# Kernel optimization log

Hardware: AMD Instinct MI355X
Metric: run time of the kernel (lower is better)

## Reference

```python
import jax, jax.numpy as jnp
import numpy as np

T = 5
EPS = 1e-05


def setup_inputs() -> dict:
    key = jax.random.key(0)
    X = jax.random.normal(key, (64, 512, 32, 32), dtype=jnp.float32)
    return {"X": X}


def reference(X):
    # IterNorm (training branch): whiten channels via Newton-Schulz inverse sqrt.
    N, C, H, W = X.shape
    x = jnp.transpose(X, (1, 0, 2, 3)).reshape(C, -1)  # [d, m], d=C, m=N*H*W
    d, m = x.shape
    mean = jnp.mean(x, axis=-1, keepdims=True)
    xc = x - mean
    I = jnp.eye(d, dtype=X.dtype)
    # Sigma = eps*I + (1/m) xc xc^T  (addmm(eps, I, 1/m, xc, xc^T))
    Sigma = EPS * I + (xc @ xc.T) / m
    rTr = 1.0 / jnp.trace(Sigma)          # (Sigma * I).sum().reciprocal()
    Sigma_N = Sigma * rTr
    P = I
    for _ in range(T):
        # P_{k+1} = 1.5*P_k - 0.5 * P_k^3 @ Sigma_N
        P = 1.5 * P - 0.5 * (P @ P @ P) @ Sigma_N
    wm = P * jnp.sqrt(rTr)                # whitening matrix ~ Sigma^{-1/2}
    xn = wm @ xc                          # [d, m]
    Xn = jnp.transpose(xn.reshape(C, N, H, W), (1, 0, 2, 3))
    return Xn
```

## Files before the change

### kernel.cpp

```cpp
#include <hip/hip_runtime.h>
#include <math.h>

#define Nn   64
#define Cc   512
#define HWs  1024
#define CHW  (Cc * HWs)
#define Mm   (Nn * HWs)
#define EPSC 1e-5f
#define NBC  128

typedef unsigned int   u32;
typedef unsigned short u16;
typedef unsigned long long u64;
typedef __attribute__((ext_vector_type(8))) short  short8;
typedef __attribute__((ext_vector_type(4))) float  floatx4;

__device__ __forceinline__ u16 f2bf(float f) {
    u32 u = __float_as_uint(f);
    u += 0x7fff + ((u >> 16) & 1);
    return (u16)(u >> 16);
}
__device__ __forceinline__ float bf2f(u16 h) {
    return __uint_as_float(((u32)h) << 16);
}

__device__ __forceinline__ void gld_lds16(const u16* g, u16* l) {
    __builtin_amdgcn_global_load_lds(
        (const __attribute__((address_space(1))) u32*)g,
        (__attribute__((address_space(3))) u32*)l, 16, 0, 0);
}

#define AUX_SC 0x11

__device__ __forceinline__ void gld_lds16_sc(const u16* g, u16* l) {
    __builtin_amdgcn_global_load_lds(
        (const __attribute__((address_space(1))) u32*)g,
        (__attribute__((address_space(3))) u32*)l, 16, 0, AUX_SC);
}
__device__ __forceinline__ void st8_sc(u16* p, u64 pk) {
    asm volatile("global_store_dwordx2 %0, %1, off sc0 sc1"
                 :: "v"(p), "v"(pk) : "memory");
}
__device__ __forceinline__ u64 pk4(const u16* h) {
    return (u64)h[0] | ((u64)h[1] << 16) | ((u64)h[2] << 32) | ((u64)h[3] << 48);
}

#define WAITV(N) asm volatile("s_waitcnt vmcnt(" #N ")" ::: "memory")
#define RAWBAR() __builtin_amdgcn_s_barrier()

__global__ __launch_bounds__(256) void convert_transpose(const float* __restrict__ X,
                                                         u16* __restrict__ Xbf,
                                                         u16* __restrict__ Xt,
                                                         float* __restrict__ meanP) {
    const int hT = blockIdx.x;
    const int h0 = hT << 6;
    const int c0 = blockIdx.y << 6;
    const int n  = blockIdx.z;
    const int t  = threadIdx.x;
    __shared__ u16   T[64][65];
    __shared__ float red[64][17];

    const float* Xn  = X   + (size_t)n * CHW;
    u16*         Xbn = Xbf + (size_t)n * CHW;
    u16*         Xtn = Xt  + (size_t)n * CHW;

    const int cl = t >> 4;
    const int h4 = (t & 15) << 2;
#pragma unroll
    for (int i = 0; i < 4; ++i) {
        const int c = cl + (i << 4);
        float4 v = *(const float4*)&Xn[(size_t)(c0 + c) * HWs + h0 + h4];
        red[c][t & 15] = v.x + v.y + v.z + v.w;
        u16 b0 = f2bf(v.x), b1 = f2bf(v.y), b2 = f2bf(v.z), b3 = f2bf(v.w);
        *(ushort4*)&Xbn[(size_t)(c0 + c) * HWs + h0 + h4] = make_ushort4(b0, b1, b2, b3);
        T[c][h4]     = b0;
        T[c][h4 + 1] = b1;
        T[c][h4 + 2] = b2;
        T[c][h4 + 3] = b3;
    }
    __syncthreads();
    const int hl = t >> 4;
    const int c4 = (t & 15) << 2;
#pragma unroll
    for (int i = 0; i < 4; ++i) {
        const int h = hl + (i << 4);
        ushort4 pk = make_ushort4(T[c4][h], T[c4 + 1][h], T[c4 + 2][h], T[c4 + 3][h]);
        *(ushort4*)&Xtn[(size_t)(h0 + h) * Cc + c0 + c4] = pk;
    }
    if (t < 64) {
        float s = 0.f;
#pragma unroll
        for (int j = 0; j < 16; ++j) s += red[t][j];
        atomicAdd(&meanP[hT * 512 + c0 + t], s);
    }
}

__global__ __launch_bounds__(256) void gram_mfma(const u16* __restrict__ Xbf,
                                                 float* __restrict__ G) {
    static const int TI[10] = {0,0,0,0,1,1,1,2,2,3};
    static const int TJ[10] = {0,1,2,3,1,2,3,2,3,3};
    const int id = blockIdx.x;
    const int q  = id >> 3;
    const int x  = q % 10;
    const int y  = (id & 7) + ((q / 10) << 3);
    const int i0 = TI[x] << 7;
    const int j0 = TJ[x] << 7;
    const int n0 = y << 1;
    const int t  = threadIdx.x;
    const int w  = t >> 6, l = t & 63;

    __shared__ u16 As[2][4096];
    __shared__ u16 Bs[2][4096];

    floatx4 acc[4][4];
#pragma unroll
    for (int mi = 0; mi < 4; ++mi)
#pragma unroll
        for (int ni = 0; ni < 4; ++ni) acc[mi][ni] = (floatx4){0.f, 0.f, 0.f, 0.f};

    const int lr = l >> 2;
    const int lc = (l & 3) << 3;
    const int wm = w >> 1, wn = w & 1;
    const int fm = l & 15, fq = l >> 4;

    auto issue = [&](int s, int bb) {
        const u16* Xn = Xbf + (size_t)(n0 + (s >> 5)) * CHW;
        const int hw  = (s & 31) << 5;
#pragma unroll
        for (int p = 0; p < 2; ++p) {
            const int g   = w * 2 + p;
            const int row = g * 16 + lr;
            gld_lds16(Xn + (size_t)(i0 + row) * HWs + hw + lc, &As[bb][g * 512]);
            gld_lds16(Xn + (size_t)(j0 + row) * HWs + hw + lc, &Bs[bb][g * 512]);
        }
    };

    issue(0, 0);
    issue(1, 1);
    for (int s = 0; s < 64; ++s) {
        if (s < 63) WAITV(4); else WAITV(0);
        RAWBAR();
        const int bb = s & 1;
        short8 a[4], b[4];
#pragma unroll
        for (int mi = 0; mi < 4; ++mi)
            a[mi] = *(const short8*)&As[bb][(wm * 64 + mi * 16 + fm) * 32 + fq * 8];
#pragma unroll
        for (int ni = 0; ni < 4; ++ni)
            b[ni] = *(const short8*)&Bs[bb][(wn * 64 + ni * 16 + fm) * 32 + fq * 8];
#pragma unroll
        for (int mi = 0; mi < 4; ++mi)
#pragma unroll
            for (int ni = 0; ni < 4; ++ni)
                acc[mi][ni] = __builtin_amdgcn_mfma_f32_16x16x32_bf16(
                    a[mi], b[ni], acc[mi][ni], 0, 0, 0);
        RAWBAR();
        if (s < 62) issue(s + 2, bb);
    }
#pragma unroll
    for (int mi = 0; mi < 4; ++mi)
#pragma unroll
        for (int ni = 0; ni < 4; ++ni)
#pragma unroll
            for (int r = 0; r < 4; ++r) {
                const int gi = i0 + wm * 64 + mi * 16 + fq * 4 + r;
                const int gj = j0 + wn * 64 + ni * 16 + fm;
                atomicAdd(&G[(size_t)gi * Cc + gj], acc[mi][ni][r]);
            }
}

__device__ __forceinline__ void gridbar(int* bar, int gen) {
    asm volatile("s_waitcnt vmcnt(0)" ::: "memory");
    __syncthreads();
    if (threadIdx.x == 0) {
        __hip_atomic_fetch_add(bar, 1, __ATOMIC_RELAXED, __HIP_MEMORY_SCOPE_AGENT);
        while (__hip_atomic_load(bar, __ATOMIC_RELAXED, __HIP_MEMORY_SCOPE_AGENT) < gen * NBC)
            __builtin_amdgcn_s_sleep(1);
    }
    __syncthreads();
}

template <int MR>
__device__ __forceinline__ void mm_bk64(const u16* Ah, const u16* Al,
                                        const u16* Bh, const u16* Bl,
                                        int i0, int j0,
                                        float alpha, const float* D, float beta,
                                        float* Cf, u16* Ch, u16* Cl, u16* S) {
    const int t = threadIdx.x, w = t >> 6, l = t & 63;
    const int wm = w >> 1, wn = w & 1, fm = l & 15, fq = l >> 4;
    const int lr = l >> 2, lc = (l & 3) << 3;
    constexpr int MI     = MR / 32;
    constexpr int OFF_AL = MR * 64;
    constexpr int OFF_BH = 2 * MR * 64;
    constexpr int OFF_BL = 2 * MR * 64 + 4096;
    constexpr int BUFSZ  = 2 * MR * 64 + 8192;

    const u16* src  = (w == 0) ? Ah : (w == 1) ? Al : (w == 2) ? Bh : Bl;
    const int rbase = (w < 2) ? i0 : j0;
    const int R     = (w < 2) ? MR : 64;
    const int OFF   = (w == 0) ? 0 : (w == 1) ? OFF_AL : (w == 2) ? OFF_BH : OFF_BL;

    floatx4 acc[MI][2];
#pragma unroll
    for (int mi = 0; mi < MI; ++mi)
#pragma unroll
        for (int ni = 0; ni < 2; ++ni) acc[mi][ni] = (floatx4){0.f, 0.f, 0.f, 0.f};

    auto issue = [&](int c, int bb) {
        u16* dst = S + bb * BUFSZ + OFF;
        const u16* sp = src + (size_t)rbase * 512 + (c << 6);
#pragma unroll
        for (int s = 0; s < 2; ++s)
#pragma unroll 4
            for (int g = 0; g < (R >> 4); ++g)
                gld_lds16_sc(sp + (size_t)(g * 16 + lr) * 512 + s * 32 + lc,
                             dst + s * R * 32 + g * 512);
    };
    auto waitL = [&](bool last) {
        if (last) { WAITV(0); return; }
        if (MR == 64) { WAITV(8); }
        else if (w < 2) { WAITV(4); } else { WAITV(8); }
    };
    auto compute = [&](int bb) {
        const u16* base = S + bb * BUFSZ;
#pragma unroll
        for (int s = 0; s < 2; ++s) {
            short8 ah[MI], al[MI], bh[2], bl[2];
#pragma unroll
            for (int mi = 0; mi < MI; ++mi) {
                const int r = wm * (MR / 2) + mi * 16 + fm;
                const int o = s * MR * 32 + r * 32 + fq * 8;
                ah[mi] = *(const short8*)&base[o];
                al[mi] = *(const short8*)&base[OFF_AL + o];
            }
#pragma unroll
            for (int ni = 0; ni < 2; ++ni) {
                const int r = wn * 32 + ni * 16 + fm;
                const int o = s * 2048 + r * 32 + fq * 8;
                bh[ni] = *(const short8*)&base[OFF_BH + o];
                bl[ni] = *(const short8*)&base[OFF_BL + o];
            }
#pragma unroll
            for (int mi = 0; mi < MI; ++mi)
#pragma unroll
                for (int ni = 0; ni < 2; ++ni) {
                    acc[mi][ni] = __builtin_amdgcn_mfma_f32_16x16x32_bf16(ah[mi], bh[ni], acc[mi][ni], 0, 0, 0);
                    acc[mi][ni] = __builtin_amdgcn_mfma_f32_16x16x32_bf16(ah[mi], bl[ni], acc[mi][ni], 0, 0, 0);
                    acc[mi][ni] = __builtin_amdgcn_mfma_f32_16x16x32_bf16(al[mi], bh[ni], acc[mi][ni], 0, 0, 0);
                }
        }
    };

    issue(0, 0);
    issue(1, 1);
    for (int c = 0; c < 8; ++c) {
        waitL(c == 7);
        RAWBAR();
        compute(c & 1);
        RAWBAR();
        if (c < 6) issue(c + 2, c & 1);
    }

#pragma unroll
    for (int mi = 0; mi < MI; ++mi)
#pragma unroll
        for (int ni = 0; ni < 2; ++ni) {
            const int gib = i0 + wm * (MR / 2) + mi * 16 + fq * 4;
            const int gj  = j0 + wn * 32 + ni * 16 + fm;
            u16 h[4], lo[4];
#pragma unroll
            for (int r4 = 0; r4 < 4; ++r4) {
                float v = alpha * acc[mi][ni][r4];
                if (D) v += beta * D[(size_t)(gib + r4) * 512 + gj];
                if (Cf) Cf[(size_t)(gib + r4) * 512 + gj] = v;
                h[r4]  = f2bf(v);
                lo[r4] = f2bf(v - bf2f(h[r4]));
            }
            st8_sc(&Ch[(size_t)gj * 512 + gib], pk4(h));
            st8_sc(&Cl[(size_t)gj * 512 + gib], pk4(lo));
        }
}

__global__ __launch_bounds__(256) void ns_chain(
    const float* G, const float* meanP, float* scal, int* bar, float* wmmv,
    u16* Sh, u16* Sl, u16* PhA, u16* PlA, u16* PhB, u16* PlB,
    u16* T2h, u16* T2l, u16* Wh, u16* Wl, float* PfA, float* PfB) {
    __shared__ u16   S[32768];
    __shared__ float meanL[512];
    __shared__ float redL[4];
    const int t = threadIdx.x, b = blockIdx.x;
    const int w = t >> 6, l = t & 63;

    float tp = 0.f;
#pragma unroll
    for (int cb = 0; cb < 2; ++cb) {
        const int c = t + (cb << 8);
        float s = 0.f;
#pragma unroll
        for (int q = 0; q < 16; ++q) s += meanP[(q << 9) + c];
        const float mc = s * (1.0f / Mm);
        meanL[c] = mc;
        tp += G[(size_t)c * 513] * (1.0f / Mm) - mc * mc;
    }
#pragma unroll
    for (int o = 32; o > 0; o >>= 1) tp += __shfl_xor(tp, o);
    if (l == 0) redL[w] = tp;
    __syncthreads();
    const float tr  = redL[0] + redL[1] + redL[2] + redL[3] + (float)Cc * EPSC;
    const float rtr = 1.0f / tr;
    const float sr  = sqrtf(rtr);
    if (b == 0 && t == 0) { scal[0] = rtr; scal[1] = sr; }

    const int R0 = (b >> 3) << 5;
    const int C0 = (b & 7) << 6;
#pragma unroll
    for (int k2 = 0; k2 < 2; ++k2) {
        const int idx4 = (k2 << 8) + t;
        const int i  = R0 + (idx4 >> 4);
        const int jb = C0 + ((idx4 & 15) << 2);
        float p1[4];
        u16 sh[4], sl[4], ph[4], pl[4];
#pragma unroll
        for (int u = 0; u < 4; ++u) {
            const int j = jb + u;
            const float g = (i <= j) ? G[((size_t)i << 9) + j] : G[((size_t)j << 9) + i];
            float sig = g * (1.0f / Mm) - meanL[i] * meanL[j];
            if (i == j) sig += EPSC;
            const float sN = sig * rtr;
            sh[u] = f2bf(sN);
            sl[u] = f2bf(sN - bf2f(sh[u]));
            p1[u] = ((i == j) ? 1.5f : 0.f) - 0.5f * sN;
            ph[u] = f2bf(p1[u]);
            pl[u] = f2bf(p1[u] - bf2f(ph[u]));
        }
        const size_t e = ((size_t)i << 9) + jb;
        st8_sc(&Sh[e],  pk4(sh));
        st8_sc(&Sl[e],  pk4(sl));
        st8_sc(&PhA[e], pk4(ph));
        st8_sc(&PlA[e], pk4(pl));
        *(float4*)&PfA[e] = make_float4(p1[0], p1[1], p1[2], p1[3]);
    }
    int gen = 0;
    gridbar(bar, ++gen);

    u16 *ph = PhA, *pl = PlA, *qh = PhB, *ql = PlB;
    float *pf = PfA, *qf = PfB;
    const int i0a = ((b & 63) >> 3) << 6, j0a = (b & 7) << 6;
    for (int it = 0; it < 4; ++it) {
        if (b < 64)
            mm_bk64<64>(ph, pl, ph, pl, i0a, j0a, 1.f, nullptr, 0.f,
                        nullptr, T2h, T2l, S);
        else
            mm_bk64<64>(ph, pl, Sh, Sl, i0a, j0a, 1.f, nullptr, 0.f,
                        nullptr, Wh, Wl, S);
        gridbar(bar, ++gen);
        mm_bk64<32>(T2h, T2l, Wh, Wl, R0, C0, -0.5f, pf, 1.5f,
                    qf, qh, ql, S);
        gridbar(bar, ++gen);
        { u16* x = ph; ph = qh; qh = x; }
        { u16* x = pl; pl = ql; ql = x; }
        { float* x = pf; pf = qf; qf = x; }
    }

    {
        const int row = R0 + (t >> 3);
        const int jb  = C0 + ((t & 7) << 3);
        float s = 0.f;
#pragma unroll
        for (int jj = 0; jj < 8; ++jj)
            s += pf[((size_t)row << 9) + jb + jj] * meanL[jb + jj];
        s += __shfl_xor(s, 1);
        s += __shfl_xor(s, 2);
        s += __shfl_xor(s, 4);
        if ((t & 7) == 0) atomicAdd(&wmmv[row], s * sr);
    }
}

__global__ __launch_bounds__(256) void whiten_mfma(const u16* __restrict__ Xt,
                                                   const u16* __restrict__ Pbf,
                                                   const float* __restrict__ wmm,
                                                   const float* __restrict__ scal,
                                                   float* __restrict__ out) {
    const int id  = blockIdx.x;
    const int m   = (id >> 3) & 3;
    const int grp = (id & 7) + ((id >> 5) << 3);
    const int c0  = m << 7;
    const int h0  = (grp & 3) << 8;
    const int n   = grp >> 2;
    const int t   = threadIdx.x;
    const int w   = t >> 6, l = t & 63;

    __shared__ char smem[49152];
    u16* As = (u16*)smem;
    u16* Bs = As + 16384;
    float* Ep = (float*)smem;

    floatx4 acc[8][4];
#pragma unroll
    for (int mi = 0; mi < 8; ++mi)
#pragma unroll
        for (int ni = 0; ni < 4; ++ni) acc[mi][ni] = (floatx4){0.f, 0.f, 0.f, 0.f};

    const int lr = l >> 2;
    const int lc = (l & 3) << 3;
    const int wm = w >> 1, wn = w & 1;
    const int fm = l & 15, fq = l >> 4;

    const u16* Xn = Xt + (size_t)n * CHW;

    auto issue = [&](int k, int bb) {
        const int kk = k << 5;
#pragma unroll
        for (int gi = 0; gi < 4; ++gi) {
            const int g = w * 4 + gi;
            gld_lds16(Xn + (size_t)(h0 + g * 16 + lr) * Cc + kk + lc,
                      &As[bb * 8192 + g * 512]);
        }
#pragma unroll
        for (int p = 0; p < 2; ++p) {
            const int g = w * 2 + p;
            gld_lds16(Pbf + (size_t)(c0 + g * 16 + lr) * Cc + kk + lc,
                      &Bs[bb * 4096 + g * 512]);
        }
    };

    issue(0, 0);
    issue(1, 1);
    for (int k = 0; k < 16; ++k) {
        if (k < 15) WAITV(6); else WAITV(0);
        RAWBAR();
        const int bb = k & 1;
        short8 a[8], b[4];
#pragma unroll
        for (int mi = 0; mi < 8; ++mi)
            a[mi] = *(const short8*)&As[bb * 8192 + (wm * 128 + mi * 16 + fm) * 32 + fq * 8];
#pragma unroll
        for (int ni = 0; ni < 4; ++ni)
            b[ni] = *(const short8*)&Bs[bb * 4096 + (wn * 64 + ni * 16 + fm) * 32 + fq * 8];
#pragma unroll
        for (int mi = 0; mi < 8; ++mi)
#pragma unroll
            for (int ni = 0; ni < 4; ++ni)
                acc[mi][ni] = __builtin_amdgcn_mfma_f32_16x16x32_bf16(
                    a[mi], b[ni], acc[mi][ni], 0, 0, 0);
        RAWBAR();
        if (k < 14) issue(k + 2, bb);
    }

    const float sr = scal[1];
    float wv[4];
#pragma unroll
    for (int ni = 0; ni < 4; ++ni) wv[ni] = wmm[c0 + wn * 64 + ni * 16 + fm];
    float* outn = out + (size_t)n * CHW;

#pragma unroll
    for (int mp = 0; mp < 4; ++mp) {
        __syncthreads();
#pragma unroll
        for (int p = 0; p < 2; ++p) {
            const int mi = mp * 2 + p;
#pragma unroll
            for (int ni = 0; ni < 4; ++ni) {
                const int row  = wn * 64 + ni * 16 + fm;
                const int slot = wm * 32 + p * 16 + fq * 4;
                floatx4 v = acc[mi][ni] * sr - wv[ni];
                *(floatx4*)&Ep[row * 68 + slot] = v;
            }
        }
        __syncthreads();
#pragma unroll
        for (int jj = 0; jj < 8; ++jj) {
            const int idx = jj * 256 + t;
            const int row = idx >> 4;
            const int s4  = (idx & 15) << 2;
            const int wmr = s4 >> 5;
            const int within = s4 & 31;
            float4 v = *(const float4*)&Ep[row * 68 + s4];
            *(float4*)&outn[(size_t)(c0 + row) * HWs + h0 + wmr * 128 + mp * 32 + within] = v;
        }
    }
}

__global__ __launch_bounds__(256) void mean_kernel(const float* __restrict__ X,
                                                   float* __restrict__ mean) {
    const int c = blockIdx.x;
    const int t = threadIdx.x;
    float s = 0.f;
    for (int n = 0; n < Nn; ++n) {
        const float4* p = (const float4*)(X + (size_t)n * CHW + (size_t)c * HWs);
        float4 v = p[t];
        s += v.x + v.y + v.z + v.w;
    }
    __shared__ float red[256];
    red[t] = s;
    __syncthreads();
    for (int o = 128; o > 0; o >>= 1) {
        if (t < o) red[t] += red[t + o];
        __syncthreads();
    }
    if (t == 0) mean[c] = red[0] * (1.0f / Mm);
}

__global__ __launch_bounds__(256) void trace_fb(const float* __restrict__ G,
                                                const float* __restrict__ mean,
                                                float* __restrict__ scal) {
    const int t = threadIdx.x;
    float s = 0.f;
    for (int i = t; i < Cc; i += 256)
        s += G[(size_t)i * Cc + i] * (1.0f / Mm) - mean[i] * mean[i];
    __shared__ float red[256];
    red[t] = s;
    __syncthreads();
    for (int o = 128; o > 0; o >>= 1) {
        if (t < o) red[t] += red[t + o];
        __syncthreads();
    }
    if (t == 0) {
        const float tr  = red[0] + (float)Cc * EPSC;
        const float rtr = 1.0f / tr;
        scal[0] = rtr;
        scal[1] = sqrtf(rtr);
    }
}

__global__ __launch_bounds__(256) void gram_kernel(const float* __restrict__ X,
                                                   float* __restrict__ G) {
    const int ti = blockIdx.x >> 3, tj = blockIdx.x & 7;
    const int i0 = ti << 6, j0 = tj << 6;
    const int n0 = blockIdx.y << 3;
    const int t  = threadIdx.x;
    const int tx = t & 15, ty = t >> 4;
    __shared__ float As[64][33];
    __shared__ float Bs[64][33];
    float acc[4][4] = {};
    const int lc = t & 31;
    const int lr0 = t >> 5;
    for (int n = n0; n < n0 + 8; ++n) {
        const float* Xn = X + (size_t)n * CHW;
        for (int hw0 = 0; hw0 < HWs; hw0 += 32) {
#pragma unroll
            for (int r = 0; r < 8; ++r) {
                const int row = lr0 + (r << 3);
                As[row][lc] = Xn[(size_t)(i0 + row) * HWs + hw0 + lc];
                Bs[row][lc] = Xn[(size_t)(j0 + row) * HWs + hw0 + lc];
            }
            __syncthreads();
#pragma unroll
            for (int k = 0; k < 32; ++k) {
                float a[4], b[4];
#pragma unroll
                for (int r = 0; r < 4; ++r) a[r] = As[(ty << 2) + r][k];
#pragma unroll
                for (int cn = 0; cn < 4; ++cn) b[cn] = Bs[(tx << 2) + cn][k];
#pragma unroll
                for (int r = 0; r < 4; ++r)
#pragma unroll
                    for (int cn = 0; cn < 4; ++cn) acc[r][cn] += a[r] * b[cn];
            }
            __syncthreads();
        }
    }
#pragma unroll
    for (int r = 0; r < 4; ++r)
#pragma unroll
        for (int cn = 0; cn < 4; ++cn)
            atomicAdd(&G[(size_t)(i0 + (ty << 2) + r) * Cc + j0 + (tx << 2) + cn],
                      acc[r][cn]);
}

__global__ __launch_bounds__(256) void sigman_full_kernel(const float* __restrict__ G,
                                                          const float* __restrict__ mean,
                                                          const float* __restrict__ scal,
                                                          float* __restrict__ S,
                                                          float* __restrict__ P) {
    const int e = blockIdx.x * 256 + threadIdx.x;
    const int i = e >> 9, j = e & 511;
    const float rtr = scal[0];
    float sig = G[e] * (1.0f / Mm) - mean[i] * mean[j];
    if (i == j) sig += EPSC;
    S[e] = sig * rtr;
    P[e] = (i == j) ? 1.f : 0.f;
}

__global__ __launch_bounds__(256) void mm512_kernel(const float* __restrict__ A,
                                                    const float* __restrict__ B,
                                                    float* __restrict__ C,
                                                    float alpha,
                                                    const float* __restrict__ D,
                                                    float beta) {
    const int ti = blockIdx.x >> 3, tj = blockIdx.x & 7;
    const int i0 = ti << 6, j0 = tj << 6;
    const int t  = threadIdx.x;
    const int tx = t & 15, ty = t >> 4;
    __shared__ float As[64][33];
    __shared__ float Bs[32][65];
    float acc[4][4] = {};
    const int lcA = t & 31, lrA = t >> 5;
    const int lcB = t & 63, lrB = t >> 6;
    for (int k0 = 0; k0 < 512; k0 += 32) {
#pragma unroll
        for (int r = 0; r < 8; ++r) {
            const int row = lrA + (r << 3);
            As[row][lcA] = A[(size_t)(i0 + row) * 512 + k0 + lcA];
        }
#pragma unroll
        for (int r = 0; r < 8; ++r) {
            const int row = lrB + (r << 2);
            Bs[row][lcB] = B[(size_t)(k0 + row) * 512 + j0 + lcB];
        }
        __syncthreads();
#pragma unroll
        for (int k = 0; k < 32; ++k) {
            float a[4], b[4];
#pragma unroll
            for (int r = 0; r < 4; ++r) a[r] = As[(ty << 2) + r][k];
#pragma unroll
            for (int cn = 0; cn < 4; ++cn) b[cn] = Bs[k][(tx << 2) + cn];
#pragma unroll
            for (int r = 0; r < 4; ++r)
#pragma unroll
                for (int cn = 0; cn < 4; ++cn) acc[r][cn] += a[r] * b[cn];
        }
        __syncthreads();
    }
#pragma unroll
    for (int r = 0; r < 4; ++r) {
        const size_t idx = (size_t)(i0 + (ty << 2) + r) * 512 + j0 + (tx << 2);
        float4 v;
        v.x = alpha * acc[r][0];
        v.y = alpha * acc[r][1];
        v.z = alpha * acc[r][2];
        v.w = alpha * acc[r][3];
        if (D) {
            const float4 d = *(const float4*)(D + idx);
            v.x += beta * d.x; v.y += beta * d.y; v.z += beta * d.z; v.w += beta * d.w;
        }
        *(float4*)(C + idx) = v;
    }
}

__global__ __launch_bounds__(128) void wmm_kernel(const float* __restrict__ P,
                                                  const float* __restrict__ mean,
                                                  const float* __restrict__ scal,
                                                  float* __restrict__ wmm) {
    const int c = blockIdx.x, t = threadIdx.x;
    float s = 0.f;
    for (int j = t; j < Cc; j += 128) s += P[(size_t)c * Cc + j] * mean[j];
    __shared__ float red[128];
    red[t] = s;
    __syncthreads();
    for (int o = 64; o > 0; o >>= 1) {
        if (t < o) red[t] += red[t + o];
        __syncthreads();
    }
    if (t == 0) wmm[c] = red[0] * scal[1];
}

__global__ __launch_bounds__(256) void whiten_kernel(const float* __restrict__ X,
                                                     const float* __restrict__ P,
                                                     const float* __restrict__ wmm,
                                                     const float* __restrict__ scal,
                                                     float* __restrict__ out) {
    const int c0 = blockIdx.x << 6;
    const int h0 = blockIdx.y << 6;
    const int n  = blockIdx.z;
    const int t  = threadIdx.x;
    const int tx = t & 15, ty = t >> 4;
    __shared__ float Ps[64][33];
    __shared__ float Xs[32][65];
    float acc[4][4] = {};
    const int lcA = t & 31, lrA = t >> 5;
    const int lcB = t & 63, lrB = t >> 6;
    const float* Xn = X + (size_t)n * CHW;
    for (int k0 = 0; k0 < 512; k0 += 32) {
#pragma unroll
        for (int r = 0; r < 8; ++r) {
            const int row = lrA + (r << 3);
            Ps[row][lcA] = P[(size_t)(c0 + row) * 512 + k0 + lcA];
        }
#pragma unroll
        for (int r = 0; r < 8; ++r) {
            const int row = lrB + (r << 2);
            Xs[row][lcB] = Xn[(size_t)(k0 + row) * HWs + h0 + lcB];
        }
        __syncthreads();
#pragma unroll
        for (int k = 0; k < 32; ++k) {
            float a[4], b[4];
#pragma unroll
            for (int r = 0; r < 4; ++r) a[r] = Ps[(ty << 2) + r][k];
#pragma unroll
            for (int cn = 0; cn < 4; ++cn) b[cn] = Xs[k][(tx << 2) + cn];
#pragma unroll
            for (int r = 0; r < 4; ++r)
#pragma unroll
                for (int cn = 0; cn < 4; ++cn) acc[r][cn] += a[r] * b[cn];
        }
        __syncthreads();
    }
    const float sr = scal[1];
#pragma unroll
    for (int r = 0; r < 4; ++r) {
        const int c = c0 + (ty << 2) + r;
        const float wv = wmm[c];
        float4 v;
        v.x = sr * acc[r][0] - wv;
        v.y = sr * acc[r][1] - wv;
        v.z = sr * acc[r][2] - wv;
        v.w = sr * acc[r][3] - wv;
        *(float4*)(out + (size_t)n * CHW + (size_t)c * HWs + h0 + (tx << 2)) = v;
    }
}

extern "C" void kernel_launch(void* const* d_in, const int* in_sizes, int n_in,
                              void* d_out, int out_size, void* d_ws, size_t ws_size,
                              hipStream_t stream) {
    const float* X = (const float*)d_in[0];
    float* out     = (float*)d_out;

    const size_t NU16 = 33554432;
    const size_t NM   = 262144;
    const size_t NEED = NU16 * 2 * 2
                      + NM * 10 * 2
                      + (NM + 8192 + 32 + 512 + 512 + 2 * NM) * 4;

    if (ws_size >= NEED) {
        u16* Xbf = (u16*)d_ws;
        u16* Xt  = Xbf + NU16;
        u16* Sh  = Xt  + NU16;
        u16* Sl  = Sh + NM;
        u16* PhA = Sl + NM;
        u16* PlA = PhA + NM;
        u16* PhB = PlA + NM;
        u16* PlB = PhB + NM;
        u16* T2h = PlB + NM;
        u16* T2l = T2h + NM;
        u16* Wh  = T2l + NM;
        u16* Wl  = Wh + NM;
        float* G     = (float*)(Wl + NM);
        float* meanP = G + NM;
        float* scal  = meanP + 8192;
        int*   bar   = (int*)(scal + 16);
        float* mean  = (float*)(bar + 16);
        float* wmm   = mean + 512;
        float* PfA   = wmm + 512;
        float* PfB   = PfA + NM;

        hipMemsetAsync(G, 0, (NM + 8192 + 32 + 1024) * sizeof(float), stream);
        convert_transpose<<<dim3(16, 8, 64), 256, 0, stream>>>(X, Xbf, Xt, meanP);
        gram_mfma<<<320, 256, 0, stream>>>(Xbf, G);
        ns_chain<<<NBC, 256, 0, stream>>>(G, meanP, scal, bar, wmm,
                                          Sh, Sl, PhA, PlA, PhB, PlB,
                                          T2h, T2l, Wh, Wl, PfA, PfB);
        whiten_mfma<<<1024, 256, 0, stream>>>(Xt, PhA, wmm, scal, out);
    } else {
        float* ws   = (float*)d_ws;
        float* mean = ws;
        float* wmm  = ws + 512;
        float* scal = ws + 1024;
        float* G    = ws + 2048;
        float* S    = G + 262144;
        float* Pa   = S + 262144;
        float* Pb   = Pa + 262144;
        float* P2   = Pb + 262144;
        float* P3   = P2 + 262144;

        mean_kernel<<<512, 256, 0, stream>>>(X, mean);
        hipMemsetAsync(G, 0, sizeof(float) * 262144, stream);
        gram_kernel<<<dim3(64, 8), 256, 0, stream>>>(X, G);
        trace_fb<<<1, 256, 0, stream>>>(G, mean, scal);
        sigman_full_kernel<<<1024, 256, 0, stream>>>(G, mean, scal, S, Pa);

        float* P  = Pa;
        float* Pn = Pb;
        for (int it = 0; it < 5; ++it) {
            mm512_kernel<<<64, 256, 0, stream>>>(P, P, P2, 1.f, nullptr, 0.f);
            mm512_kernel<<<64, 256, 0, stream>>>(P2, P, P3, 1.f, nullptr, 0.f);
            mm512_kernel<<<64, 256, 0, stream>>>(P3, S, Pn, -0.5f, P, 1.5f);
            float* tmp = P; P = Pn; Pn = tmp;
        }

        wmm_kernel<<<512, 128, 0, stream>>>(P, mean, scal, wmm);
        whiten_kernel<<<dim3(8, 16, 64), 256, 0, stream>>>(X, P, wmm, scal, out);
    }
}
```

Baseline: 458.7 us.

## Use 128x128 tiles and 32 blocks in Newton-Schulz iteration kernel

The persistent Newton-Schulz kernel drops from 128 blocks with 64x64/32x64 tiles to 32 blocks that each compute 128x128 output tiles, doubling the LDS buffer. Fewer blocks make each grid barrier cheaper, and the larger tiles give more reuse per LDS load. The cost is far less parallelism on a large GPU: the second matmul runs on only 16 blocks, which adds serial compute per block. The transpose LDS tile is also padded and aligned so each thread writes it with one vectorised store.

```diff
diff --git a/kernel.cpp b/kernel.cpp
--- a/kernel.cpp
+++ b/kernel.cpp
@@ -7,7 +7,7 @@
 #define CHW  (Cc * HWs)
 #define Mm   (Nn * HWs)
 #define EPSC 1e-5f
-#define NBC  128
+#define NBC  32
 
 typedef unsigned int   u32;
 typedef unsigned short u16;
@@ -57,7 +57,7 @@
     const int c0 = blockIdx.y << 6;
     const int n  = blockIdx.z;
     const int t  = threadIdx.x;
-    __shared__ u16   T[64][65];
+    __shared__ __align__(16) u16 T[64][68];
     __shared__ float red[64][17];
 
     const float* Xn  = X   + (size_t)n * CHW;
@@ -73,10 +73,7 @@
         red[c][t & 15] = v.x + v.y + v.z + v.w;
         u16 b0 = f2bf(v.x), b1 = f2bf(v.y), b2 = f2bf(v.z), b3 = f2bf(v.w);
         *(ushort4*)&Xbn[(size_t)(c0 + c) * HWs + h0 + h4] = make_ushort4(b0, b1, b2, b3);
-        T[c][h4]     = b0;
-        T[c][h4 + 1] = b1;
-        T[c][h4 + 2] = b2;
-        T[c][h4 + 3] = b3;
+        *(ushort4*)&T[c][h4] = make_ushort4(b0, b1, b2, b3);
     }
     __syncthreads();
     const int hl = t >> 4;
@@ -180,70 +177,58 @@
     __syncthreads();
 }
 
-template <int MR>
-__device__ __forceinline__ void mm_bk64(const u16* Ah, const u16* Al,
-                                        const u16* Bh, const u16* Bl,
-                                        int i0, int j0,
-                                        float alpha, const float* D, float beta,
-                                        float* Cf, u16* Ch, u16* Cl, u16* S) {
+__device__ __forceinline__ void mm128(const u16* Ah, const u16* Al,
+                                      const u16* Bh, const u16* Bl,
+                                      int i0, int j0,
+                                      float alpha, const float* D, float beta,
+                                      float* Cf, u16* Ch, u16* Cl, u16* S) {
     const int t = threadIdx.x, w = t >> 6, l = t & 63;
     const int wm = w >> 1, wn = w & 1, fm = l & 15, fq = l >> 4;
     const int lr = l >> 2, lc = (l & 3) << 3;
-    constexpr int MI     = MR / 32;
-    constexpr int OFF_AL = MR * 64;
-    constexpr int OFF_BH = 2 * MR * 64;
-    constexpr int OFF_BL = 2 * MR * 64 + 4096;
-    constexpr int BUFSZ  = 2 * MR * 64 + 8192;
 
     const u16* src  = (w == 0) ? Ah : (w == 1) ? Al : (w == 2) ? Bh : Bl;
     const int rbase = (w < 2) ? i0 : j0;
-    const int R     = (w < 2) ? MR : 64;
-    const int OFF   = (w == 0) ? 0 : (w == 1) ? OFF_AL : (w == 2) ? OFF_BH : OFF_BL;
-
-    floatx4 acc[MI][2];
-#pragma unroll
-    for (int mi = 0; mi < MI; ++mi)
-#pragma unroll
-        for (int ni = 0; ni < 2; ++ni) acc[mi][ni] = (floatx4){0.f, 0.f, 0.f, 0.f};
+    const int OFF   = w << 13;
+
+    floatx4 acc[4][4];
+#pragma unroll
+    for (int mi = 0; mi < 4; ++mi)
+#pragma unroll
+        for (int ni = 0; ni < 4; ++ni) acc[mi][ni] = (floatx4){0.f, 0.f, 0.f, 0.f};
 
     auto issue = [&](int c, int bb) {
-        u16* dst = S + bb * BUFSZ + OFF;
+        u16* dst = S + (bb << 15) + OFF;
         const u16* sp = src + (size_t)rbase * 512 + (c << 6);
 #pragma unroll
         for (int s = 0; s < 2; ++s)
-#pragma unroll 4
-            for (int g = 0; g < (R >> 4); ++g)
+#pragma unroll
+            for (int g = 0; g < 8; ++g)
                 gld_lds16_sc(sp + (size_t)(g * 16 + lr) * 512 + s * 32 + lc,
-                             dst + s * R * 32 + g * 512);
-    };
-    auto waitL = [&](bool last) {
-        if (last) { WAITV(0); return; }
-        if (MR == 64) { WAITV(8); }
-        else if (w < 2) { WAITV(4); } else { WAITV(8); }
+                             dst + s * 4096 + g * 512);
     };
     auto compute = [&](int bb) {
-        const u16* base = S + bb * BUFSZ;
+        const u16* base = S + (bb << 15);
 #pragma unroll
         for (int s = 0; s < 2; ++s) {
-            short8 ah[MI], al[MI], bh[2], bl[2];
-#pragma unroll
-            for (int mi = 0; mi < MI; ++mi) {
-                const int r = wm * (MR / 2) + mi * 16 + fm;
-                const int o = s * MR * 32 + r * 32 + fq * 8;
+            short8 ah[4], al[4], bh[4], bl[4];
+#pragma unroll
+            for (int mi = 0; mi < 4; ++mi) {
+                const int r = wm * 64 + mi * 16 + fm;
+                const int o = s * 4096 + r * 32 + fq * 8;
                 ah[mi] = *(const short8*)&base[o];
-                al[mi] = *(const short8*)&base[OFF_AL + o];
-            }
-#pragma unroll
-            for (int ni = 0; ni < 2; ++ni) {
-                const int r = wn * 32 + ni * 16 + fm;
-                const int o = s * 2048 + r * 32 + fq * 8;
-                bh[ni] = *(const short8*)&base[OFF_BH + o];
-                bl[ni] = *(const short8*)&base[OFF_BL + o];
-            }
-#pragma unroll
-            for (int mi = 0; mi < MI; ++mi)
-#pragma unroll
-                for (int ni = 0; ni < 2; ++ni) {
+                al[mi] = *(const short8*)&base[8192 + o];
+            }
+#pragma unroll
+            for (int ni = 0; ni < 4; ++ni) {
+                const int r = wn * 64 + ni * 16 + fm;
+                const int o = s * 4096 + r * 32 + fq * 8;
+                bh[ni] = *(const short8*)&base[16384 + o];
+                bl[ni] = *(const short8*)&base[24576 + o];
+            }
+#pragma unroll
+            for (int mi = 0; mi < 4; ++mi)
+#pragma unroll
+                for (int ni = 0; ni < 4; ++ni) {
                     acc[mi][ni] = __builtin_amdgcn_mfma_f32_16x16x32_bf16(ah[mi], bh[ni], acc[mi][ni], 0, 0, 0);
                     acc[mi][ni] = __builtin_amdgcn_mfma_f32_16x16x32_bf16(ah[mi], bl[ni], acc[mi][ni], 0, 0, 0);
                     acc[mi][ni] = __builtin_amdgcn_mfma_f32_16x16x32_bf16(al[mi], bh[ni], acc[mi][ni], 0, 0, 0);
@@ -254,7 +239,7 @@
     issue(0, 0);
     issue(1, 1);
     for (int c = 0; c < 8; ++c) {
-        waitL(c == 7);
+        if (c < 7) WAITV(16); else WAITV(0);
         RAWBAR();
         compute(c & 1);
         RAWBAR();
@@ -262,11 +247,11 @@
     }
 
 #pragma unroll
-    for (int mi = 0; mi < MI; ++mi)
-#pragma unroll
-        for (int ni = 0; ni < 2; ++ni) {
-            const int gib = i0 + wm * (MR / 2) + mi * 16 + fq * 4;
-            const int gj  = j0 + wn * 32 + ni * 16 + fm;
+    for (int mi = 0; mi < 4; ++mi)
+#pragma unroll
+        for (int ni = 0; ni < 4; ++ni) {
+            const int gib = i0 + wm * 64 + mi * 16 + fq * 4;
+            const int gj  = j0 + wn * 64 + ni * 16 + fm;
             u16 h[4], lo[4];
 #pragma unroll
             for (int r4 = 0; r4 < 4; ++r4) {
@@ -285,7 +270,7 @@
     const float* G, const float* meanP, float* scal, int* bar, float* wmmv,
     u16* Sh, u16* Sl, u16* PhA, u16* PlA, u16* PhB, u16* PlB,
     u16* T2h, u16* T2l, u16* Wh, u16* Wl, float* PfA, float* PfB) {
-    __shared__ u16   S[32768];
+    __shared__ u16   S[65536];
     __shared__ float meanL[512];
     __shared__ float redL[4];
     const int t = threadIdx.x, b = blockIdx.x;
@@ -311,68 +296,86 @@
     const float sr  = sqrtf(rtr);
     if (b == 0 && t == 0) { scal[0] = rtr; scal[1] = sr; }
 
-    const int R0 = (b >> 3) << 5;
-    const int C0 = (b & 7) << 6;
-#pragma unroll
-    for (int k2 = 0; k2 < 2; ++k2) {
-        const int idx4 = (k2 << 8) + t;
-        const int i  = R0 + (idx4 >> 4);
-        const int jb = C0 + ((idx4 & 15) << 2);
-        float p1[4];
-        u16 sh[4], sl[4], ph[4], pl[4];
-#pragma unroll
-        for (int u = 0; u < 4; ++u) {
-            const int j = jb + u;
-            const float g = (i <= j) ? G[((size_t)i << 9) + j] : G[((size_t)j << 9) + i];
-            float sig = g * (1.0f / Mm) - meanL[i] * meanL[j];
-            if (i == j) sig += EPSC;
-            const float sN = sig * rtr;
-            sh[u] = f2bf(sN);
-            sl[u] = f2bf(sN - bf2f(sh[u]));
-            p1[u] = ((i == j) ? 1.5f : 0.f) - 0.5f * sN;
-            ph[u] = f2bf(p1[u]);
-            pl[u] = f2bf(p1[u] - bf2f(ph[u]));
-        }
-        const size_t e = ((size_t)i << 9) + jb;
-        st8_sc(&Sh[e],  pk4(sh));
-        st8_sc(&Sl[e],  pk4(sl));
-        st8_sc(&PhA[e], pk4(ph));
-        st8_sc(&PlA[e], pk4(pl));
-        *(float4*)&PfA[e] = make_float4(p1[0], p1[1], p1[2], p1[3]);
+    {
+        const int Rb = b << 4;
+#pragma unroll
+        for (int k2 = 0; k2 < 8; ++k2) {
+            const int idx4 = (k2 << 8) + t;
+            const int i  = Rb + (idx4 >> 7);
+            const int jb = (idx4 & 127) << 2;
+            u16 sh[4], sl[4], ph[4], pl[4];
+#pragma unroll
+            for (int u = 0; u < 4; ++u) {
+                const int j = jb + u;
+                const float g = (i <= j) ? G[((size_t)i << 9) + j] : G[((size_t)j << 9) + i];
+                float sig = g * (1.0f / Mm) - meanL[i] * meanL[j];
+                if (i == j) sig += EPSC;
+                const float sN = sig * rtr;
+                sh[u] = f2bf(sN);
+                sl[u] = f2bf(sN - bf2f(sh[u]));
+                const float p1 = ((i == j) ? 1.5f : 0.f) - 0.5f * sN;
+                ph[u] = f2bf(p1);
+                pl[u] = f2bf(p1 - bf2f(ph[u]));
+            }
+            const size_t e = ((size_t)i << 9) + jb;
+            st8_sc(&Sh[e],  pk4(sh));
+            st8_sc(&Sl[e],  pk4(sl));
+            st8_sc(&PhA[e], pk4(ph));
+            st8_sc(&PlA[e], pk4(pl));
+        }
+    }
+    const int R0 = (b >> 2) << 7;
+    const int C0 = (b & 3) << 7;
+    if (b < 16) {
+#pragma unroll
+        for (int k2 = 0; k2 < 16; ++k2) {
+            const int idx4 = (k2 << 8) + t;
+            const int i  = R0 + (idx4 >> 5);
+            const int jb = C0 + ((idx4 & 31) << 2);
+            float p1[4];
+#pragma unroll
+            for (int u = 0; u < 4; ++u) {
+                const int j = jb + u;
+                const float g = (i <= j) ? G[((size_t)i << 9) + j] : G[((size_t)j << 9) + i];
+                float sig = g * (1.0f / Mm) - meanL[i] * meanL[j];
+                if (i == j) sig += EPSC;
+                const float sN = sig * rtr;
+                p1[u] = ((i == j) ? 1.5f : 0.f) - 0.5f * sN;
+            }
+            *(float4*)&PfA[((size_t)i << 9) + jb] = make_float4(p1[0], p1[1], p1[2], p1[3]);
+        }
     }
     int gen = 0;
     gridbar(bar, ++gen);
 
     u16 *ph = PhA, *pl = PlA, *qh = PhB, *ql = PlB;
     float *pf = PfA, *qf = PfB;
-    const int i0a = ((b & 63) >> 3) << 6, j0a = (b & 7) << 6;
     for (int it = 0; it < 4; ++it) {
-        if (b < 64)
-            mm_bk64<64>(ph, pl, ph, pl, i0a, j0a, 1.f, nullptr, 0.f,
-                        nullptr, T2h, T2l, S);
+        if (b < 16)
+            mm128(ph, pl, ph, pl, (b >> 2) << 7, (b & 3) << 7, 1.f, nullptr, 0.f,
+                  nullptr, T2h, T2l, S);
         else
-            mm_bk64<64>(ph, pl, Sh, Sl, i0a, j0a, 1.f, nullptr, 0.f,
-                        nullptr, Wh, Wl, S);
+            mm128(ph, pl, Sh, Sl, ((b - 16) >> 2) << 7, ((b - 16) & 3) << 7,
+                  1.f, nullptr, 0.f, nullptr, Wh, Wl, S);
         gridbar(bar, ++gen);
-        mm_bk64<32>(T2h, T2l, Wh, Wl, R0, C0, -0.5f, pf, 1.5f,
-                    qf, qh, ql, S);
+        if (b < 16)
+            mm128(T2h, T2l, Wh, Wl, R0, C0, -0.5f, pf, 1.5f,
+                  qf, qh, ql, S);
         gridbar(bar, ++gen);
         { u16* x = ph; ph = qh; qh = x; }
         { u16* x = pl; pl = ql; ql = x; }
         { float* x = pf; pf = qf; qf = x; }
     }
 
-    {
-        const int row = R0 + (t >> 3);
-        const int jb  = C0 + ((t & 7) << 3);
+    if (b < 16) {
+        const int row = R0 + (t >> 1);
+        const int jb  = C0 + ((t & 1) << 6);
         float s = 0.f;
 #pragma unroll
-        for (int jj = 0; jj < 8; ++jj)
+        for (int jj = 0; jj < 64; ++jj)
             s += pf[((size_t)row << 9) + jb + jj] * meanL[jb + jj];
         s += __shfl_xor(s, 1);
-        s += __shfl_xor(s, 2);
-        s += __shfl_xor(s, 4);
-        if ((t & 7) == 0) atomicAdd(&wmmv[row], s * sr);
+        if ((t & 1) == 0) atomicAdd(&wmmv[row], s * sr);
     }
 }
 
```

After: 607.5 us. +32.4%, slower.
